# Kernel optimization log

Hardware: AMD Instinct MI355X
Metric: run time of the kernel (lower is better)

The kernel has to match this reference:

```python
import jax, jax.numpy as jnp
import numpy as np

B, T, IN, N, D, H, R, C = 1024, 50, 784, 128, 40, 200, 4, 5
GAMMA = 0.95  # usage decay (standard LRUA)


def setup_inputs() -> dict:
    key = jax.random.key(0)
    ks = jax.random.split(key, 9)
    xdim = IN + C + R * D  # controller input: [x, offset_label, read_vectors]

    def u(k, shape, s=0.1):
        return jax.random.uniform(k, shape, jnp.float32, -s, s)

    return {
        "images": jax.random.normal(ks[0], (B, T, IN), jnp.float32),
        "labels": jax.random.randint(ks[1], (B, T), 0, C),
        "Wx": u(ks[2], (xdim, 4 * H)),
        "Wh": u(ks[3], (H, 4 * H)),
        "b_lstm": u(ks[4], (4 * H,)),
        "Wp": u(ks[5], (H, R * (D + 1))),
        "bp": u(ks[6], (R * (D + 1),)),
        "Wc": u(ks[7], (H + R * D, C)),
        "bc": u(ks[8], (C,)),
    }


def _forward(images, labels_oh, Wx, Wh, b_lstm, Wp, bp, Wc, bc):
    # offset targets: labels shifted right by one timestep, zeros at t=0
    offset = jnp.concatenate([jnp.zeros_like(labels_oh[:, :1]), labels_oh[:, :-1]], axis=1)
    inp = jnp.concatenate([images, offset], axis=2)  # [B, T, IN+C]

    M0 = jnp.full((B, N, D), 1e-6, jnp.float32)
    r0 = jnp.full((B, R * D), 1e-6, jnp.float32)
    h0 = jnp.zeros((B, H), jnp.float32)
    c0 = jnp.zeros((B, H), jnp.float32)
    wu0 = jax.nn.one_hot(jnp.zeros((B,), jnp.int32), N)
    wr0 = jnp.tile(jax.nn.one_hot(jnp.zeros((B,), jnp.int32), N)[:, None, :], (1, R, 1))

    def step(carry, x_t):
        M, r, h, c, wu, wr = carry
        # LSTM controller
        ctrl_in = jnp.concatenate([x_t, r], axis=-1)
        gates = ctrl_in @ Wx + h @ Wh + b_lstm
        i, f, g, o = jnp.split(gates, 4, axis=-1)
        c_new = jax.nn.sigmoid(f) * c + jax.nn.sigmoid(i) * jnp.tanh(g)
        h_new = jax.nn.sigmoid(o) * jnp.tanh(c_new)
        # per-head key + interpolation gate
        p = (h_new @ Wp + bp).reshape(B, R, D + 1)
        k = jnp.tanh(p[..., :D])            # [B, R, D]
        sigma = jax.nn.sigmoid(p[..., D:])  # [B, R, 1]
        # least-used addressing from previous usage weights
        _, lu_idx = jax.lax.top_k(-wu, R)                   # R least-used slots
        w_lu = jax.nn.one_hot(lu_idx, N).sum(axis=1)        # [B, N]
        # cosine-similarity content addressing -> read weights
        kn = k / (jnp.linalg.norm(k, axis=-1, keepdims=True) + 1e-8)
        Mn = M / (jnp.linalg.norm(M, axis=-1, keepdims=True) + 1e-8)
        w_r = jax.nn.softmax(jnp.einsum('brd,bnd->brn', kn, Mn), axis=-1)  # [B,R,N]
        # write weights: interpolate prev read and least-used
        w_w = sigma * wr + (1.0 - sigma) * w_lu[:, None, :]
        wu_new = GAMMA * wu + w_r.sum(axis=1) + w_w.sum(axis=1)
        # erase least-used slot, then additive write of keys
        M_erased = M * (1.0 - jax.nn.one_hot(lu_idx[:, -1], N))[:, :, None]
        M_new = M_erased + jnp.einsum('brn,brd->bnd', w_w, k)
        # read from updated memory
        r_new = jnp.einsum('brn,bnd->brd', w_r, M_new).reshape(B, R * D)
        out = jnp.concatenate([h_new, r_new], axis=-1)
        logits = out @ Wc + bc
        return (M_new, r_new, h_new, c_new, wu_new, w_r), logits

    _, logits = jax.lax.scan(step, (M0, r0, h0, c0, wu0, wr0), jnp.swapaxes(inp, 0, 1))
    return jnp.swapaxes(logits, 0, 1)  # [B, T, C]


def reference(images, labels, Wx, Wh, b_lstm, Wp, bp, Wc, bc):
    labels_oh = jax.nn.one_hot(labels, C, dtype=jnp.float32)  # [B,T,C]
    logits = _forward(images, labels_oh, Wx, Wh, b_lstm, Wp, bp, Wc, bc)
    probs = jax.nn.softmax(logits, axis=2)
    pred = jnp.argmax(probs, axis=2).reshape(-1)
    out = probs.reshape(-1, C)
    # faithful to original: CrossEntropyLoss applied to already-softmaxed probs with soft targets
    loss = jnp.mean(-jnp.sum(labels_oh.reshape(-1, C) * jax.nn.log_softmax(out, axis=-1), axis=-1))
    tgt = labels.reshape(-1)
    acc = jnp.mean((pred == tgt).astype(jnp.float32))
    return out, loss, acc
```

## Files before the change

kernel.cpp:

```cpp
#include <hip/hip_runtime.h>
#include <hip/hip_bf16.h>
#include <math.h>

#define B_  1024
#define T_  50
#define IN_ 784
#define N_  128
#define D_  40
#define H_  200
#define R_  4
#define C_  5
#define GAMMA_ 0.95f
#define G4H_ 800
#define PDIM_ 164
#define RD_ 160
#define OUTF_ 360
#define MSZ_ 5120
#define MST_ 42
#define KP_ 800

#define AKB_ 24
#define BKB_ 36
#define WXP_N 643072
#define W2P_N (BKB_ * G4H_ * 32)
#define APK_N (AKB_ * B_ * 32)

typedef __bf16 bf16x8 __attribute__((ext_vector_type(8)));
typedef __bf16 bf16x4 __attribute__((ext_vector_type(4)));
typedef float  fx4    __attribute__((ext_vector_type(4)));

__device__ __forceinline__ float sigmoidf_(float x) { return 1.f / (1.f + expf(-x)); }

__device__ __forceinline__ void load_lds16(const void* g, void* l) {
    __builtin_amdgcn_global_load_lds(
        (const __attribute__((address_space(1))) unsigned int*)g,
        (__attribute__((address_space(3))) unsigned int*)l, 16, 0, 0);
}

__global__ __launch_bounds__(256) void pack_kernel(
    const float* __restrict__ Wx, const float* __restrict__ Wh,
    const float* __restrict__ Wp,
    __bf16* __restrict__ WxP, __bf16* __restrict__ W2P, float* __restrict__ WpT)
{
    int idx = blockIdx.x * 256 + threadIdx.x;
    if (idx < WXP_N) {
        int kb = idx / 25600, rem = idx - kb * 25600;
        int n = rem >> 5, q8 = rem & 31;
        int k = kb * 32 + q8;
        WxP[idx] = (k < IN_ && kb < 25) ? (__bf16)Wx[(size_t)k * G4H_ + n] : (__bf16)0.0f;
    }
    if (idx < W2P_N) {
        int kb = idx / (G4H_ * 32), rem = idx - kb * (G4H_ * 32);
        int n = rem >> 5, q8 = rem & 31;
        int kl = (kb < 12 ? kb : (kb < 24 ? kb - 12 : kb - 24)) * 32 + q8;
        __bf16 o = (__bf16)0.0f;
        if (kl < OUTF_) {
            float v = (kl < H_) ? Wh[(size_t)kl * G4H_ + n]
                                : Wx[(size_t)(789 + kl - H_) * G4H_ + n];
            __bf16 hi = (__bf16)v;
            o = (kb < 24) ? hi : (__bf16)(v - (float)hi);
        }
        W2P[idx] = o;
    }
    if (idx < PDIM_ * H_) {
        int r = idx / H_, k = idx - r * H_;
        WpT[idx] = Wp[(size_t)k * PDIM_ + r];
    }
}

__global__ void init_kernel(float* Cst, float* Mg, float* wug, float* wrg,
                            __bf16* Apack, float* scal)
{
    size_t i = (size_t)blockIdx.x * blockDim.x + threadIdx.x;
    size_t stride = (size_t)gridDim.x * blockDim.x;
    for (size_t j = i; j < (size_t)B_ * MSZ_; j += stride) Mg[j] = 1e-6f;
    for (size_t j = i; j < (size_t)B_ * H_; j += stride) Cst[j] = 0.f;
    for (size_t j = i; j < (size_t)B_ * N_; j += stride) wug[j] = ((j & (N_ - 1)) == 0) ? 1.f : 0.f;
    for (size_t j = i; j < (size_t)B_ * R_ * N_; j += stride) wrg[j] = ((j & (N_ - 1)) == 0) ? 1.f : 0.f;
    for (size_t j = i; j < (size_t)APK_N; j += stride) {
        int kb = (int)(j >> 15);
        int q8 = (int)(j & 31);
        int kl = (kb % 12) * 32 + q8;
        float v = (kl >= H_ && kl < OUTF_) ? 1e-6f : 0.f;
        __bf16 hi = (__bf16)v;
        Apack[j] = (kb < 12) ? hi : (__bf16)(v - (float)hi);
    }
    if (i < 2) scal[i] = 0.f;
}

__global__ __launch_bounds__(256) void img_convert(
    const float* __restrict__ images, __bf16* __restrict__ img)
{
    long long gi = (long long)blockIdx.x * 256 + threadIdx.x;
    if (gi * 4 >= (long long)T_ * B_ * KP_) return;
    long long m = (gi * 4) / KP_;
    int k = (int)((gi * 4) - m * KP_);
    int t = (int)(m >> 10), b = (int)(m & (B_ - 1));
    bf16x4 o;
    if (k < IN_) {
        const float4 v = *(const float4*)&images[((size_t)b * T_ + t) * IN_ + k];
        o[0] = (__bf16)v.x; o[1] = (__bf16)v.y; o[2] = (__bf16)v.z; o[3] = (__bf16)v.w;
    } else {
        o[0] = o[1] = o[2] = o[3] = (__bf16)0.0f;
    }
    *(bf16x4*)&img[(size_t)m * KP_ + k] = o;
}

__global__ __launch_bounds__(256) void gx_mfma(
    const __bf16* __restrict__ img, const __bf16* __restrict__ WxP,
    const int* __restrict__ labels, const float* __restrict__ Wx,
    const float* __restrict__ b_lstm, float* __restrict__ Gx)
{
    __shared__ __bf16 A_lds[4096];
    __shared__ __bf16 B_lds[5120];

    const int tid  = threadIdx.x;
    const int lane = tid & 63, w = tid >> 6;
    const int quad = lane >> 4, ln = lane & 15;
    const int swzl = (ln & 3) ^ ((ln >> 2) & 3);
    const int row0 = blockIdx.x * 128;
    const int n0   = blockIdx.y * 160;
    const int mw   = (w >> 1) * 64;
    const int nw   = (w & 1) * 80;

    fx4 acc[4][5];
    #pragma unroll
    for (int i = 0; i < 4; i++)
        #pragma unroll
        for (int j = 0; j < 5; j++) acc[i][j] = (fx4)0.0f;

    for (int kb = 0; kb < 25; kb++) {
        #pragma unroll
        for (int p = 0; p < 2; p++) {
            int cc = p * 256 + tid;
            int m = cc >> 2, c = cc & 3;
            int q = c ^ ((m & 3) ^ ((m >> 2) & 3));
            load_lds16(img + (size_t)(row0 + m) * KP_ + kb * 32 + q * 8,
                       &A_lds[(size_t)(p * 256 + w * 64) * 8]);
        }
        #pragma unroll
        for (int p = 0; p < 3; p++) {
            if (p * 4 + w < 10) {
                int cc = p * 256 + tid;
                int n = cc >> 2, c = cc & 3;
                int q = c ^ ((n & 3) ^ ((n >> 2) & 3));
                load_lds16(WxP + ((size_t)kb * G4H_ + n0 + n) * 32 + q * 8,
                           &B_lds[(size_t)(p * 256 + w * 64) * 8]);
            }
        }
        __syncthreads();

        bf16x8 a[4], bb[5];
        #pragma unroll
        for (int mi = 0; mi < 4; mi++)
            a[mi] = *(const bf16x8*)&A_lds[((mw + mi * 16 + ln) * 4 + (quad ^ swzl)) * 8];
        #pragma unroll
        for (int ni = 0; ni < 5; ni++)
            bb[ni] = *(const bf16x8*)&B_lds[((nw + ni * 16 + ln) * 4 + (quad ^ swzl)) * 8];
        #pragma unroll
        for (int mi = 0; mi < 4; mi++)
            #pragma unroll
            for (int ni = 0; ni < 5; ni++)
                acc[mi][ni] = __builtin_amdgcn_mfma_f32_16x16x32_bf16(a[mi], bb[ni], acc[mi][ni], 0, 0, 0);
        __syncthreads();
    }

    #pragma unroll
    for (int mi = 0; mi < 4; mi++) {
        #pragma unroll
        for (int rr = 0; rr < 4; rr++) {
            int row = row0 + mw + mi * 16 + quad * 4 + rr;
            int t = row >> 10, b = row & (B_ - 1);
            int lbl = (t > 0) ? labels[b * T_ + t - 1] : -1;
            #pragma unroll
            for (int ni = 0; ni < 5; ni++) {
                int col = n0 + nw + ni * 16 + ln;
                float add = b_lstm[col];
                if (lbl >= 0) add += Wx[(size_t)(IN_ + lbl) * G4H_ + col];
                Gx[(size_t)row * G4H_ + col] = acc[mi][ni][rr] + add;
            }
        }
    }
}

__global__ __launch_bounds__(256) void rec_mfma(
    const __bf16* __restrict__ Apack, const __bf16* __restrict__ W2P,
    const float* __restrict__ Gxt, float* __restrict__ gates)
{
    __shared__ __bf16 A_lds[8192];
    __shared__ __bf16 B_lds[4096];

    const int tid  = threadIdx.x;
    const int lane = tid & 63, w = tid >> 6;
    const int quad = lane >> 4, ln = lane & 15;
    const int swzl = (ln & 3) ^ ((ln >> 2) & 3);
    const int row0 = blockIdx.x * 64;
    const int col0 = blockIdx.y * 32;
    const int mw   = (w >> 1) * 32;
    const int nw   = (w & 1) * 16;

    fx4 acc[2];
    acc[0] = (fx4)0.0f; acc[1] = (fx4)0.0f;

    for (int it = 0; it < 9; it++) {
        #pragma unroll
        for (int p = 0; p < 4; p++) {
            int cc = p * 256 + tid;
            int kbl = cc >> 8, row = (cc >> 2) & 63, c = cc & 3;
            int q = c ^ ((row & 3) ^ ((row >> 2) & 3));
            int kbg = it * 4 + kbl;
            int kba = (kbg < AKB_) ? kbg : kbg - AKB_;
            load_lds16(Apack + ((size_t)kba * B_ + row0 + row) * 32 + q * 8,
                       &A_lds[(size_t)(p * 256 + w * 64) * 8]);
        }
        #pragma unroll
        for (int p = 0; p < 2; p++) {
            int cc = p * 256 + tid;
            int kbl = cc >> 7, n = (cc >> 2) & 31, c = cc & 3;
            int q = c ^ ((n & 3) ^ ((n >> 2) & 3));
            int kbg = it * 4 + kbl;
            load_lds16(W2P + ((size_t)kbg * G4H_ + col0 + n) * 32 + q * 8,
                       &B_lds[(size_t)(p * 256 + w * 64) * 8]);
        }
        __syncthreads();

        #pragma unroll
        for (int s = 0; s < 4; s++) {
            bf16x8 a0 = *(const bf16x8*)&A_lds[((s * 64 + mw + ln) * 4 + (quad ^ swzl)) * 8];
            bf16x8 a1 = *(const bf16x8*)&A_lds[((s * 64 + mw + 16 + ln) * 4 + (quad ^ swzl)) * 8];
            bf16x8 b0 = *(const bf16x8*)&B_lds[((s * 32 + nw + ln) * 4 + (quad ^ swzl)) * 8];
            acc[0] = __builtin_amdgcn_mfma_f32_16x16x32_bf16(a0, b0, acc[0], 0, 0, 0);
            acc[1] = __builtin_amdgcn_mfma_f32_16x16x32_bf16(a1, b0, acc[1], 0, 0, 0);
        }
        __syncthreads();
    }

    #pragma unroll
    for (int mi = 0; mi < 2; mi++) {
        #pragma unroll
        for (int rr = 0; rr < 4; rr++) {
            int row = row0 + mw + mi * 16 + quad * 4 + rr;
            int col = col0 + nw + ln;
            gates[(size_t)row * G4H_ + col] = acc[mi][rr] + Gxt[(size_t)row * G4H_ + col];
        }
    }
}

__global__ __launch_bounds__(256) void step_kernel(
    const float* __restrict__ gates, __bf16* __restrict__ Apack, float* __restrict__ Cst,
    float* __restrict__ Mg, float* __restrict__ wug, float* __restrict__ wrg,
    const float* __restrict__ WpT, const float* __restrict__ bp,
    const float* __restrict__ Wc, const float* __restrict__ bc,
    float* __restrict__ out, int t)
{
    const int b = blockIdx.x;
    const int tid = threadIdx.x;
    const int lane = tid & 63, w = tid >> 6;
    const int nn = tid >> 1, dh = tid & 1, d0 = dh * 20;

    __shared__ float M_s[N_ * MST_];
    __shared__ float h_s[H_];
    __shared__ float k_s[RD_];
    __shared__ float sig_s[R_];
    __shared__ float wu_s[N_];
    __shared__ int   lu_s[R_];
    __shared__ float wrn_s[R_ * N_];
    __shared__ float ww_s[R_ * N_];
    __shared__ float rn_s[RD_];
    __shared__ float red[160];

    float m[20];

    if (tid < H_) {
        const float gi = gates[(size_t)b * G4H_ + tid];
        const float gf = gates[(size_t)b * G4H_ + H_ + tid];
        const float gg = gates[(size_t)b * G4H_ + 2 * H_ + tid];
        const float go = gates[(size_t)b * G4H_ + 3 * H_ + tid];
        const float c_old = Cst[b * H_ + tid];
        const float cn = sigmoidf_(gf) * c_old + sigmoidf_(gi) * tanhf(gg);
        const float hn = sigmoidf_(go) * tanhf(cn);
        Cst[b * H_ + tid] = cn;
        h_s[tid] = hn;
        __bf16 hi = (__bf16)hn;
        __bf16 lo = (__bf16)(hn - (float)hi);
        const int kb = tid >> 5, q8 = tid & 31;
        Apack[((size_t)kb * B_ + b) * 32 + q8] = hi;
        Apack[((size_t)(kb + 12) * B_ + b) * 32 + q8] = lo;
    }
    if (tid < N_) wu_s[tid] = wug[b * N_ + tid];
    {
        const float* src = Mg + (size_t)b * MSZ_ + nn * D_ + d0;
        #pragma unroll
        for (int j = 0; j < 20; j += 4) {
            float4 v = *(const float4*)&src[j];
            m[j] = v.x; m[j + 1] = v.y; m[j + 2] = v.z; m[j + 3] = v.w;
        }
    }
    __syncthreads();

    if (tid < PDIM_) {
        float acc = bp[tid];
        const float* wr = WpT + (size_t)tid * H_;
        #pragma unroll 5
        for (int k2 = 0; k2 < H_; k2 += 4) {
            float4 wv = *(const float4*)&wr[k2];
            float4 hv = *(const float4*)&h_s[k2];
            acc += hv.x * wv.x + hv.y * wv.y + hv.z * wv.z + hv.w * wv.w;
        }
        int r = tid / (D_ + 1), d = tid - r * (D_ + 1);
        if (d < D_) k_s[r * D_ + d] = tanhf(acc);
        else        sig_s[r] = sigmoidf_(acc);
    }
    if (w == 3) {
        float v0 = wu_s[lane], v1 = wu_s[lane + 64];
        #pragma unroll
        for (int r4 = 0; r4 < R_; r4++) {
            float v; int idx;
            if (v1 < v0) { v = v1; idx = lane + 64; } else { v = v0; idx = lane; }
            #pragma unroll
            for (int off = 32; off > 0; off >>= 1) {
                float ov = __shfl_down(v, off);
                int   oi = __shfl_down(idx, off);
                if (ov < v || (ov == v && oi < idx)) { v = ov; idx = oi; }
            }
            int bi = __shfl(idx, 0);
            if (lane == 0) lu_s[r4] = bi;
            if (lane == bi) v0 = 3.0e38f;
            if (lane + 64 == bi) v1 = 3.0e38f;
        }
    }
    __syncthreads();

    {
        float nr = 0.f;
        #pragma unroll
        for (int j = 0; j < 20; j++) nr += m[j] * m[j];
        float dt[4];
        #pragma unroll
        for (int r = 0; r < 4; r++) {
            float s = 0.f;
            const float* kr = &k_s[r * D_ + d0];
            #pragma unroll
            for (int j = 0; j < 20; j += 4) {
                float4 kv = *(const float4*)&kr[j];
                s += m[j] * kv.x + m[j + 1] * kv.y + m[j + 2] * kv.z + m[j + 3] * kv.w;
            }
            dt[r] = s;
        }
        nr += __shfl_xor(nr, 1);
        #pragma unroll
        for (int r = 0; r < 4; r++) dt[r] += __shfl_xor(dt[r], 1);
        const float den = sqrtf(nr) + 1e-8f;
        if (dh == 0) { wrn_s[nn] = dt[0] / den;          wrn_s[N_ + nn] = dt[1] / den; }
        else         { wrn_s[2 * N_ + nn] = dt[2] / den; wrn_s[3 * N_ + nn] = dt[3] / den; }
    }
    __syncthreads();

    {
        const int r = w;
        float kv = (lane < D_) ? k_s[r * D_ + lane] * k_s[r * D_ + lane] : 0.f;
        #pragma unroll
        for (int off = 32; off > 0; off >>= 1) kv += __shfl_xor(kv, off);
        const float kinv = 1.f / (sqrtf(kv) + 1e-8f);

        const int n0i = lane, n1i = lane + 64;
        float s0 = wrn_s[r * N_ + n0i] * kinv;
        float s1 = wrn_s[r * N_ + n1i] * kinv;
        const float sg = sig_s[r];
        float wlu0 = (n0i == lu_s[0] || n0i == lu_s[1] || n0i == lu_s[2] || n0i == lu_s[3]) ? 1.f : 0.f;
        float wlu1 = (n1i == lu_s[0] || n1i == lu_s[1] || n1i == lu_s[2] || n1i == lu_s[3]) ? 1.f : 0.f;
        ww_s[r * N_ + n0i] = sg * wrg[(size_t)b * (R_ * N_) + r * N_ + n0i] + (1.f - sg) * wlu0;
        ww_s[r * N_ + n1i] = sg * wrg[(size_t)b * (R_ * N_) + r * N_ + n1i] + (1.f - sg) * wlu1;
        float mx = fmaxf(s0, s1);
        #pragma unroll
        for (int off = 32; off > 0; off >>= 1) mx = fmaxf(mx, __shfl_xor(mx, off));
        float e0 = expf(s0 - mx), e1 = expf(s1 - mx);
        float sm = e0 + e1;
        #pragma unroll
        for (int off = 32; off > 0; off >>= 1) sm += __shfl_xor(sm, off);
        const float inv = 1.f / sm;
        e0 *= inv; e1 *= inv;
        wrn_s[r * N_ + n0i] = e0;
        wrn_s[r * N_ + n1i] = e1;
        wrg[(size_t)b * (R_ * N_) + r * N_ + n0i] = e0;
        wrg[(size_t)b * (R_ * N_) + r * N_ + n1i] = e1;
    }
    __syncthreads();

    if (tid < N_) {
        float acc = GAMMA_ * wu_s[tid];
        #pragma unroll
        for (int r = 0; r < R_; r++) acc += wrn_s[r * N_ + tid] + ww_s[r * N_ + tid];
        wug[b * N_ + tid] = acc;
    }
    {
        const int lu4 = lu_s[3];
        if (nn == lu4) {
            #pragma unroll
            for (int j = 0; j < 20; j++) m[j] = 0.f;
        }
        float wgt[4];
        #pragma unroll
        for (int r = 0; r < 4; r++) wgt[r] = ww_s[r * N_ + nn];
        #pragma unroll
        for (int r = 0; r < 4; r++) {
            const float* kr = &k_s[r * D_ + d0];
            const float g = wgt[r];
            #pragma unroll
            for (int j = 0; j < 20; j += 4) {
                float4 kv = *(const float4*)&kr[j];
                m[j]     += g * kv.x;
                m[j + 1] += g * kv.y;
                m[j + 2] += g * kv.z;
                m[j + 3] += g * kv.w;
            }
        }
        float* mrow = &M_s[nn * MST_ + d0];
        float* gdst = Mg + (size_t)b * MSZ_ + nn * D_ + d0;
        #pragma unroll
        for (int j = 0; j < 20; j += 4) {
            *(float2*)&mrow[j]     = make_float2(m[j], m[j + 1]);
            *(float2*)&mrow[j + 2] = make_float2(m[j + 2], m[j + 3]);
            *(float4*)&gdst[j]     = make_float4(m[j], m[j + 1], m[j + 2], m[j + 3]);
        }
    }
    __syncthreads();

    if (tid < RD_) {
        const int r = tid / D_, d = tid - r * D_;
        const float* wrow = &wrn_s[r * N_];
        float a0 = 0.f, a1 = 0.f, a2 = 0.f, a3 = 0.f;
        #pragma unroll 8
        for (int n2 = 0; n2 < N_; n2 += 4) {
            float4 wv = *(const float4*)&wrow[n2];
            a0 += wv.x * M_s[(n2 + 0) * MST_ + d];
            a1 += wv.y * M_s[(n2 + 1) * MST_ + d];
            a2 += wv.z * M_s[(n2 + 2) * MST_ + d];
            a3 += wv.w * M_s[(n2 + 3) * MST_ + d];
        }
        const float acc = (a0 + a1) + (a2 + a3);
        rn_s[tid] = acc;
        __bf16 hi = (__bf16)acc;
        __bf16 lo = (__bf16)(acc - (float)hi);
        const int kp = H_ + tid;
        const int kb = kp >> 5, q8 = kp & 31;
        Apack[((size_t)kb * B_ + b) * 32 + q8] = hi;
        Apack[((size_t)(kb + 12) * B_ + b) * 32 + q8] = lo;
    }
    __syncthreads();

    if (tid < 160) {
        int c = tid >> 5, seg = tid & 31;
        float acc = 0.f;
        for (int j = seg; j < OUTF_; j += 32) {
            float v = (j < H_) ? h_s[j] : rn_s[j - H_];
            acc += v * Wc[j * C_ + c];
        }
        red[tid] = acc;
    }
    __syncthreads();

    if (w == 0) {
        float lg = 0.f;
        if (lane < C_) {
            lg = bc[lane];
            #pragma unroll
            for (int s = 0; s < 32; s++) lg += red[lane * 32 + s];
        }
        float l0 = __shfl(lg, 0), l1 = __shfl(lg, 1), l2 = __shfl(lg, 2);
        float l3 = __shfl(lg, 3), l4 = __shfl(lg, 4);
        if (lane == 0) {
            float mx = fmaxf(fmaxf(fmaxf(l0, l1), fmaxf(l2, l3)), l4);
            float e0 = expf(l0 - mx), e1 = expf(l1 - mx), e2 = expf(l2 - mx);
            float e3 = expf(l3 - mx), e4 = expf(l4 - mx);
            float inv = 1.f / (e0 + e1 + e2 + e3 + e4);
            float* o = out + ((size_t)b * T_ + t) * C_;
            o[0] = e0 * inv; o[1] = e1 * inv; o[2] = e2 * inv; o[3] = e3 * inv; o[4] = e4 * inv;
        }
    }
}

__global__ __launch_bounds__(256) void loss_kernel(
    const float* __restrict__ out, const int* __restrict__ labels, float* __restrict__ la)
{
    int row = blockIdx.x * 256 + threadIdx.x;
    float li = 0.f, ai = 0.f;
    if (row < B_ * T_) {
        float p[C_];
        #pragma unroll
        for (int c = 0; c < C_; c++) p[c] = out[(size_t)row * C_ + c];
        int tgt = labels[row];
        float mx = p[0];
        #pragma unroll
        for (int c = 1; c < C_; c++) mx = fmaxf(mx, p[c]);
        float sm = 0.f;
        #pragma unroll
        for (int c = 0; c < C_; c++) sm += expf(p[c] - mx);
        li = (mx + logf(sm) - p[tgt]) * (1.f / (B_ * T_));
        int pred = 0; float bv = p[0];
        #pragma unroll
        for (int c = 1; c < C_; c++) if (p[c] > bv) { bv = p[c]; pred = c; }
        ai = (pred == tgt) ? (1.f / (B_ * T_)) : 0.f;
    }
    for (int off = 32; off > 0; off >>= 1) {
        li += __shfl_down(li, off);
        ai += __shfl_down(ai, off);
    }
    if ((threadIdx.x & 63) == 0) {
        atomicAdd(&la[0], li);
        atomicAdd(&la[1], ai);
    }
}

extern "C" void kernel_launch(void* const* d_in, const int* in_sizes, int n_in,
                              void* d_out, int out_size, void* d_ws, size_t ws_size,
                              hipStream_t stream)
{
    const float* images = (const float*)d_in[0];
    const int*   labels = (const int*)d_in[1];
    const float* Wx     = (const float*)d_in[2];
    const float* Wh     = (const float*)d_in[3];
    const float* b_lstm = (const float*)d_in[4];
    const float* Wp     = (const float*)d_in[5];
    const float* bp     = (const float*)d_in[6];
    const float* Wc     = (const float*)d_in[7];
    const float* bc     = (const float*)d_in[8];
    float* out = (float*)d_out;

    float* ws = (float*)d_ws;
    float* gates = ws;
    float* Cst   = gates + (size_t)B_ * G4H_;
    float* Mg    = Cst   + (size_t)B_ * H_;
    float* wug   = Mg    + (size_t)B_ * MSZ_;
    float* wrg   = wug   + (size_t)B_ * N_;
    float* Gx    = wrg   + (size_t)B_ * R_ * N_;
    __bf16* imgb = (__bf16*)(Gx + (size_t)T_ * B_ * G4H_);
    __bf16* WxP  = imgb + (size_t)T_ * B_ * KP_;
    __bf16* W2P  = WxP  + (size_t)WXP_N;
    __bf16* Apack = W2P + (size_t)W2P_N;
    float*  WpT  = (float*)(Apack + (size_t)APK_N);

    pack_kernel<<<(W2P_N + 255) / 256, 256, 0, stream>>>(Wx, Wh, Wp, WxP, W2P, WpT);
    init_kernel<<<1024, 256, 0, stream>>>(Cst, Mg, wug, wrg, Apack, out + (size_t)B_ * T_ * C_);

    img_convert<<<(int)(((long long)T_ * B_ * KP_ / 4 + 255) / 256), 256, 0, stream>>>(images, imgb);
    gx_mfma<<<dim3(T_ * B_ / 128, 5), 256, 0, stream>>>(imgb, WxP, labels, Wx, b_lstm, Gx);

    for (int t = 0; t < T_; t++) {
        rec_mfma<<<dim3(B_ / 64, G4H_ / 32), 256, 0, stream>>>(
            Apack, W2P, Gx + (size_t)t * B_ * G4H_, gates);
        step_kernel<<<B_, 256, 0, stream>>>(
            gates, Apack, Cst, Mg, wug, wrg, WpT, bp, Wc, bc, out, t);
    }

    loss_kernel<<<(B_ * T_) / 256, 256, 0, stream>>>(out, labels, out + (size_t)B_ * T_ * C_);
}
```

Baseline: 2.204 ms.

## Fuse per-timestep recurrent GEMM and step kernels into persistent kernel with grid barrier

Replaces the 100 per-timestep launches (rec_mfma plus step_kernel) with one persistent kernel of 1024 blocks that loops over time and separates the phases with a hierarchical atomic grid barrier. Memory state, cell state and read weights stay in registers and LDS across steps instead of being reloaded from global memory. This targets launch overhead and state round-trips, but needs all 1024 blocks co-resident (4 per CU, checked through an occupancy query with a fallback). It adds two grid-wide barriers per step and leaves 624 blocks idle during the GEMM phase.

Result: no change. 2.205 ms (+0.1%).

```diff
diff --git a/kernel.cpp b/kernel.cpp
--- a/kernel.cpp
+++ b/kernel.cpp
@@ -25,6 +25,9 @@
 #define W2P_N (BKB_ * G4H_ * 32)
 #define APK_N (AKB_ * B_ * 32)
 
+#define NBLK_ 1024
+#define BAR_N (34 * 32)
+
 typedef __bf16 bf16x8 __attribute__((ext_vector_type(8)));
 typedef __bf16 bf16x4 __attribute__((ext_vector_type(4)));
 typedef float  fx4    __attribute__((ext_vector_type(4)));
@@ -35,6 +38,32 @@
     __builtin_amdgcn_global_load_lds(
         (const __attribute__((address_space(1))) unsigned int*)g,
         (__attribute__((address_space(3))) unsigned int*)l, 16, 0, 0);
+}
+
+__device__ __forceinline__ void grid_barrier(unsigned* bar, int tid) {
+    __threadfence();
+    __syncthreads();
+    if (tid == 0) {
+        unsigned* leaf   = &bar[(blockIdx.x & 31) * 32];
+        unsigned* master = &bar[32 * 32];
+        unsigned* gen    = &bar[33 * 32];
+        unsigned g0 = __hip_atomic_load(gen, __ATOMIC_RELAXED, __HIP_MEMORY_SCOPE_AGENT);
+        unsigned a = __hip_atomic_fetch_add(leaf, 1u, __ATOMIC_ACQ_REL, __HIP_MEMORY_SCOPE_AGENT);
+        if (a == 31u) {
+            unsigned b2 = __hip_atomic_fetch_add(master, 1u, __ATOMIC_ACQ_REL, __HIP_MEMORY_SCOPE_AGENT);
+            if (b2 == 31u) {
+                #pragma unroll
+                for (int i = 0; i < 32; i++)
+                    __hip_atomic_store(&bar[i * 32], 0u, __ATOMIC_RELAXED, __HIP_MEMORY_SCOPE_AGENT);
+                __hip_atomic_store(master, 0u, __ATOMIC_RELAXED, __HIP_MEMORY_SCOPE_AGENT);
+                __hip_atomic_fetch_add(gen, 1u, __ATOMIC_RELEASE, __HIP_MEMORY_SCOPE_AGENT);
+            }
+        }
+        while (__hip_atomic_load(gen, __ATOMIC_RELAXED, __HIP_MEMORY_SCOPE_AGENT) == g0)
+            __builtin_amdgcn_s_sleep(8);
+    }
+    __syncthreads();
+    __threadfence();
 }
 
 __global__ __launch_bounds__(256) void pack_kernel(
@@ -69,7 +98,7 @@
 }
 
 __global__ void init_kernel(float* Cst, float* Mg, float* wug, float* wrg,
-                            __bf16* Apack, float* scal)
+                            __bf16* Apack, float* scal, unsigned* bar)
 {
     size_t i = (size_t)blockIdx.x * blockDim.x + threadIdx.x;
     size_t stride = (size_t)gridDim.x * blockDim.x;
@@ -85,6 +114,7 @@
         __bf16 hi = (__bf16)v;
         Apack[j] = (kb < 12) ? hi : (__bf16)(v - (float)hi);
     }
+    for (size_t j = i; j < (size_t)BAR_N; j += stride) bar[j] = 0u;
     if (i < 2) scal[i] = 0.f;
 }
 
@@ -480,6 +510,294 @@
     }
 }
 
+__global__ __launch_bounds__(256, 4) void fused_loop(
+    __bf16* __restrict__ Apack, const __bf16* __restrict__ W2P,
+    const float* __restrict__ Gx, float* __restrict__ gates,
+    const float* __restrict__ WpT, const float* __restrict__ bp,
+    const float* __restrict__ Wc, const float* __restrict__ bc,
+    float* __restrict__ out, unsigned* bar)
+{
+    __shared__ float Msh[6144];
+    __shared__ float h_s[H_];
+    __shared__ float k_s[RD_];
+    __shared__ float sig_s[R_];
+    __shared__ float wu_s[N_];
+    __shared__ int   lu_s[R_];
+    __shared__ float wrn_s[R_ * N_];
+    __shared__ float ww_s[R_ * N_];
+    __shared__ float rn_s[RD_];
+    __shared__ float red[160];
+
+    const int tid  = threadIdx.x;
+    const int lane = tid & 63, w = tid >> 6;
+    const int b    = blockIdx.x;
+    const int nn = tid >> 1, dh = tid & 1, d0 = dh * 20;
+    const int quad = lane >> 4, ln = lane & 15;
+    const int swzl = (ln & 3) ^ ((ln >> 2) & 3);
+
+    float m[20];
+    #pragma unroll
+    for (int j = 0; j < 20; j++) m[j] = 1e-6f;
+    float c_reg = 0.f;
+    float wr0 = (lane == 0) ? 1.f : 0.f;
+    float wr1 = 0.f;
+    if (tid < N_) wu_s[tid] = (tid == 0) ? 1.f : 0.f;
+    __syncthreads();
+
+    const int row0 = (b & 15) * 64;
+    const int col0 = (b >> 4) * 32;
+    const int mw   = (w >> 1) * 32;
+    const int nw   = (w & 1) * 16;
+    __bf16* A_lds = (__bf16*)Msh;
+    __bf16* B_lds = (__bf16*)Msh + 8192;
+    float*  M_s   = Msh;
+
+    for (int t = 0; t < T_; t++) {
+        if (b < 400) {
+            fx4 acc0 = (fx4)0.0f, acc1 = (fx4)0.0f;
+            for (int it = 0; it < 9; it++) {
+                #pragma unroll
+                for (int p = 0; p < 4; p++) {
+                    int cc = p * 256 + tid;
+                    int kbl = cc >> 8, row = (cc >> 2) & 63, c = cc & 3;
+                    int q = c ^ ((row & 3) ^ ((row >> 2) & 3));
+                    int kbg = it * 4 + kbl;
+                    int kba = (kbg < AKB_) ? kbg : kbg - AKB_;
+                    load_lds16(Apack + ((size_t)kba * B_ + row0 + row) * 32 + q * 8,
+                               &A_lds[(size_t)(p * 256 + w * 64) * 8]);
+                }
+                #pragma unroll
+                for (int p = 0; p < 2; p++) {
+                    int cc = p * 256 + tid;
+                    int kbl = cc >> 7, n = (cc >> 2) & 31, c = cc & 3;
+                    int q = c ^ ((n & 3) ^ ((n >> 2) & 3));
+                    int kbg = it * 4 + kbl;
+                    load_lds16(W2P + ((size_t)kbg * G4H_ + col0 + n) * 32 + q * 8,
+                               &B_lds[(size_t)(p * 256 + w * 64) * 8]);
+                }
+                __syncthreads();
+                #pragma unroll
+                for (int s = 0; s < 4; s++) {
+                    bf16x8 a0 = *(const bf16x8*)&A_lds[((s * 64 + mw + ln) * 4 + (quad ^ swzl)) * 8];
+                    bf16x8 a1 = *(const bf16x8*)&A_lds[((s * 64 + mw + 16 + ln) * 4 + (quad ^ swzl)) * 8];
+                    bf16x8 b0 = *(const bf16x8*)&B_lds[((s * 32 + nw + ln) * 4 + (quad ^ swzl)) * 8];
+                    acc0 = __builtin_amdgcn_mfma_f32_16x16x32_bf16(a0, b0, acc0, 0, 0, 0);
+                    acc1 = __builtin_amdgcn_mfma_f32_16x16x32_bf16(a1, b0, acc1, 0, 0, 0);
+                }
+                __syncthreads();
+            }
+            const float* Gxt = Gx + (size_t)t * B_ * G4H_;
+            #pragma unroll
+            for (int mi = 0; mi < 2; mi++) {
+                fx4 acc = mi ? acc1 : acc0;
+                #pragma unroll
+                for (int rr = 0; rr < 4; rr++) {
+                    int row = row0 + mw + mi * 16 + quad * 4 + rr;
+                    int col = col0 + nw + ln;
+                    gates[(size_t)row * G4H_ + col] = acc[rr] + Gxt[(size_t)row * G4H_ + col];
+                }
+            }
+        }
+        grid_barrier(bar, tid);
+
+        if (tid < H_) {
+            const float gi = gates[(size_t)b * G4H_ + tid];
+            const float gf = gates[(size_t)b * G4H_ + H_ + tid];
+            const float gg = gates[(size_t)b * G4H_ + 2 * H_ + tid];
+            const float go = gates[(size_t)b * G4H_ + 3 * H_ + tid];
+            const float cn = sigmoidf_(gf) * c_reg + sigmoidf_(gi) * tanhf(gg);
+            const float hn = sigmoidf_(go) * tanhf(cn);
+            c_reg = cn;
+            h_s[tid] = hn;
+            __bf16 hi = (__bf16)hn;
+            __bf16 lo = (__bf16)(hn - (float)hi);
+            const int kb = tid >> 5, q8 = tid & 31;
+            Apack[((size_t)kb * B_ + b) * 32 + q8] = hi;
+            Apack[((size_t)(kb + 12) * B_ + b) * 32 + q8] = lo;
+        }
+        __syncthreads();
+
+        if (tid < PDIM_) {
+            float acc = bp[tid];
+            const float* wr = WpT + (size_t)tid * H_;
+            #pragma unroll 5
+            for (int k2 = 0; k2 < H_; k2 += 4) {
+                float4 wv = *(const float4*)&wr[k2];
+                float4 hv = *(const float4*)&h_s[k2];
+                acc += hv.x * wv.x + hv.y * wv.y + hv.z * wv.z + hv.w * wv.w;
+            }
+            int r = tid / (D_ + 1), d = tid - r * (D_ + 1);
+            if (d < D_) k_s[r * D_ + d] = tanhf(acc);
+            else        sig_s[r] = sigmoidf_(acc);
+        }
+        if (w == 3) {
+            float v0 = wu_s[lane], v1 = wu_s[lane + 64];
+            #pragma unroll
+            for (int r4 = 0; r4 < R_; r4++) {
+                float v; int idx;
+                if (v1 < v0) { v = v1; idx = lane + 64; } else { v = v0; idx = lane; }
+                #pragma unroll
+                for (int off = 32; off > 0; off >>= 1) {
+                    float ov = __shfl_down(v, off);
+                    int   oi = __shfl_down(idx, off);
+                    if (ov < v || (ov == v && oi < idx)) { v = ov; idx = oi; }
+                }
+                int bi = __shfl(idx, 0);
+                if (lane == 0) lu_s[r4] = bi;
+                if (lane == bi) v0 = 3.0e38f;
+                if (lane + 64 == bi) v1 = 3.0e38f;
+            }
+        }
+        __syncthreads();
+
+        {
+            float nr = 0.f;
+            #pragma unroll
+            for (int j = 0; j < 20; j++) nr += m[j] * m[j];
+            float dt[4];
+            #pragma unroll
+            for (int r = 0; r < 4; r++) {
+                float s = 0.f;
+                const float* kr = &k_s[r * D_ + d0];
+                #pragma unroll
+                for (int j = 0; j < 20; j += 4) {
+                    float4 kv = *(const float4*)&kr[j];
+                    s += m[j] * kv.x + m[j + 1] * kv.y + m[j + 2] * kv.z + m[j + 3] * kv.w;
+                }
+                dt[r] = s;
+            }
+            nr += __shfl_xor(nr, 1);
+            #pragma unroll
+            for (int r = 0; r < 4; r++) dt[r] += __shfl_xor(dt[r], 1);
+            const float den = sqrtf(nr) + 1e-8f;
+            if (dh == 0) { wrn_s[nn] = dt[0] / den;          wrn_s[N_ + nn] = dt[1] / den; }
+            else         { wrn_s[2 * N_ + nn] = dt[2] / den; wrn_s[3 * N_ + nn] = dt[3] / den; }
+        }
+        __syncthreads();
+
+        {
+            const int r = w;
+            float kv = (lane < D_) ? k_s[r * D_ + lane] * k_s[r * D_ + lane] : 0.f;
+            #pragma unroll
+            for (int off = 32; off > 0; off >>= 1) kv += __shfl_xor(kv, off);
+            const float kinv = 1.f / (sqrtf(kv) + 1e-8f);
+
+            const int n0i = lane, n1i = lane + 64;
+            float s0 = wrn_s[r * N_ + n0i] * kinv;
+            float s1 = wrn_s[r * N_ + n1i] * kinv;
+            const float sg = sig_s[r];
+            float wlu0 = (n0i == lu_s[0] || n0i == lu_s[1] || n0i == lu_s[2] || n0i == lu_s[3]) ? 1.f : 0.f;
+            float wlu1 = (n1i == lu_s[0] || n1i == lu_s[1] || n1i == lu_s[2] || n1i == lu_s[3]) ? 1.f : 0.f;
+            ww_s[r * N_ + n0i] = sg * wr0 + (1.f - sg) * wlu0;
+            ww_s[r * N_ + n1i] = sg * wr1 + (1.f - sg) * wlu1;
+            float mx = fmaxf(s0, s1);
+            #pragma unroll
+            for (int off = 32; off > 0; off >>= 1) mx = fmaxf(mx, __shfl_xor(mx, off));
+            float e0 = expf(s0 - mx), e1 = expf(s1 - mx);
+            float sm = e0 + e1;
+            #pragma unroll
+            for (int off = 32; off > 0; off >>= 1) sm += __shfl_xor(sm, off);
+            const float inv = 1.f / sm;
+            e0 *= inv; e1 *= inv;
+            wrn_s[r * N_ + n0i] = e0;
+            wrn_s[r * N_ + n1i] = e1;
+            wr0 = e0; wr1 = e1;
+        }
+        __syncthreads();
+
+        if (tid < N_) {
+            float acc = GAMMA_ * wu_s[tid];
+            #pragma unroll
+            for (int r = 0; r < R_; r++) acc += wrn_s[r * N_ + tid] + ww_s[r * N_ + tid];
+            wu_s[tid] = acc;
+        }
+        {
+            const int lu4 = lu_s[3];
+            if (nn == lu4) {
+                #pragma unroll
+                for (int j = 0; j < 20; j++) m[j] = 0.f;
+            }
+            float wgt[4];
+            #pragma unroll
+            for (int r = 0; r < 4; r++) wgt[r] = ww_s[r * N_ + nn];
+            #pragma unroll
+            for (int r = 0; r < 4; r++) {
+                const float* kr = &k_s[r * D_ + d0];
+                const float g = wgt[r];
+                #pragma unroll
+                for (int j = 0; j < 20; j += 4) {
+                    float4 kv = *(const float4*)&kr[j];
+                    m[j]     += g * kv.x;
+                    m[j + 1] += g * kv.y;
+                    m[j + 2] += g * kv.z;
+                    m[j + 3] += g * kv.w;
+                }
+            }
+            float* mrow = &M_s[nn * MST_ + d0];
+            #pragma unroll
+            for (int j = 0; j < 20; j += 4) {
+                *(float2*)&mrow[j]     = make_float2(m[j], m[j + 1]);
+                *(float2*)&mrow[j + 2] = make_float2(m[j + 2], m[j + 3]);
+            }
+        }
+        __syncthreads();
+
+        if (tid < RD_) {
+            const int r = tid / D_, d = tid - r * D_;
+            const float* wrow = &wrn_s[r * N_];
+            float a0 = 0.f, a1 = 0.f, a2 = 0.f, a3 = 0.f;
+            #pragma unroll 8
+            for (int n2 = 0; n2 < N_; n2 += 4) {
+                float4 wv = *(const float4*)&wrow[n2];
+                a0 += wv.x * M_s[(n2 + 0) * MST_ + d];
+                a1 += wv.y * M_s[(n2 + 1) * MST_ + d];
+                a2 += wv.z * M_s[(n2 + 2) * MST_ + d];
+                a3 += wv.w * M_s[(n2 + 3) * MST_ + d];
+            }
+            const float acc = (a0 + a1) + (a2 + a3);
+            rn_s[tid] = acc;
+            __bf16 hi = (__bf16)acc;
+            __bf16 lo = (__bf16)(acc - (float)hi);
+            const int kp = H_ + tid;
+            const int kb = kp >> 5, q8 = kp & 31;
+            Apack[((size_t)kb * B_ + b) * 32 + q8] = hi;
+            Apack[((size_t)(kb + 12) * B_ + b) * 32 + q8] = lo;
+        }
+        __syncthreads();
+
+        if (tid < 160) {
+            int c = tid >> 5, seg = tid & 31;
+            float acc = 0.f;
+            for (int j = seg; j < OUTF_; j += 32) {
+                float v = (j < H_) ? h_s[j] : rn_s[j - H_];
+                acc += v * Wc[j * C_ + c];
+            }
+            red[tid] = acc;
+        }
+        __syncthreads();
+
+        if (w == 0) {
+            float lg = 0.f;
+            if (lane < C_) {
+                lg = bc[lane];
+                #pragma unroll
+                for (int s = 0; s < 32; s++) lg += red[lane * 32 + s];
+            }
+            float l0 = __shfl(lg, 0), l1 = __shfl(lg, 1), l2 = __shfl(lg, 2);
+            float l3 = __shfl(lg, 3), l4 = __shfl(lg, 4);
+            if (lane == 0) {
+                float mx = fmaxf(fmaxf(fmaxf(l0, l1), fmaxf(l2, l3)), l4);
+                float e0 = expf(l0 - mx), e1 = expf(l1 - mx), e2 = expf(l2 - mx);
+                float e3 = expf(l3 - mx), e4 = expf(l4 - mx);
+                float inv = 1.f / (e0 + e1 + e2 + e3 + e4);
+                float* o = out + ((size_t)b * T_ + t) * C_;
+                o[0] = e0 * inv; o[1] = e1 * inv; o[2] = e2 * inv; o[3] = e3 * inv; o[4] = e4 * inv;
+            }
+        }
+        grid_barrier(bar, tid);
+    }
+}
+
 __global__ __launch_bounds__(256) void loss_kernel(
     const float* __restrict__ out, const int* __restrict__ labels, float* __restrict__ la)
 {
@@ -539,18 +857,27 @@
     __bf16* W2P  = WxP  + (size_t)WXP_N;
     __bf16* Apack = W2P + (size_t)W2P_N;
     float*  WpT  = (float*)(Apack + (size_t)APK_N);
+    unsigned* bar = (unsigned*)(WpT + (size_t)PDIM_ * H_);
 
     pack_kernel<<<(W2P_N + 255) / 256, 256, 0, stream>>>(Wx, Wh, Wp, WxP, W2P, WpT);
-    init_kernel<<<1024, 256, 0, stream>>>(Cst, Mg, wug, wrg, Apack, out + (size_t)B_ * T_ * C_);
+    init_kernel<<<1024, 256, 0, stream>>>(Cst, Mg, wug, wrg, Apack, out + (size_t)B_ * T_ * C_, bar);
 
     img_convert<<<(int)(((long long)T_ * B_ * KP_ / 4 + 255) / 256), 256, 0, stream>>>(images, imgb);
     gx_mfma<<<dim3(T_ * B_ / 128, 5), 256, 0, stream>>>(imgb, WxP, labels, Wx, b_lstm, Gx);
 
-    for (int t = 0; t < T_; t++) {
-        rec_mfma<<<dim3(B_ / 64, G4H_ / 32), 256, 0, stream>>>(
-            Apack, W2P, Gx + (size_t)t * B_ * G4H_, gates);
-        step_kernel<<<B_, 256, 0, stream>>>(
-            gates, Apack, Cst, Mg, wug, wrg, WpT, bp, Wc, bc, out, t);
+    int blocksPerCU = 0;
+    hipError_t qerr = hipOccupancyMaxActiveBlocksPerMultiprocessor(
+        &blocksPerCU, fused_loop, 256, 0);
+    if (qerr == hipSuccess && blocksPerCU >= 4) {
+        fused_loop<<<NBLK_, 256, 0, stream>>>(
+            Apack, W2P, Gx, gates, WpT, bp, Wc, bc, out, bar);
+    } else {
+        for (int t = 0; t < T_; t++) {
+            rec_mfma<<<dim3(B_ / 64, G4H_ / 32), 256, 0, stream>>>(
+                Apack, W2P, Gx + (size_t)t * B_ * G4H_, gates);
+            step_kernel<<<B_, 256, 0, stream>>>(
+                gates, Apack, Cst, Mg, wug, wrg, WpT, bp, Wc, bc, out, t);
+        }
     }
 
     loss_kernel<<<(B_ * T_) / 256, 256, 0, stream>>>(out, labels, out + (size_t)B_ * T_ * C_);
```
